# Optimization experiments

Hardware: AMD Instinct MI355X
Metric: run time of the kernel (lower is better)

## Reference

```python
import jax, jax.numpy as jnp
import numpy as np

IN_FEATURES = 512
OUT_FEATURES = 512
BATCH = 1024


def setup_inputs() -> dict:
    key = jax.random.key(0)
    k_x, k_w = jax.random.split(key)
    X = jax.random.normal(k_x, (BATCH, IN_FEATURES), dtype=jnp.float32)
    # xavier_uniform init for W [out, in]: U(-a, a), a = sqrt(6/(fan_in+fan_out))
    a = np.sqrt(6.0 / (IN_FEATURES + OUT_FEATURES)).astype(np.float32)
    W = jax.random.uniform(k_w, (OUT_FEATURES, IN_FEATURES), dtype=jnp.float32,
                           minval=-a, maxval=a)
    return {"X": X, "W": W}


def reference(X, W):
    # Tropical (min-plus) linear layer:
    #   out[b, o] = min_i ( X[b, i] + W[o, i] )
    # Broadcast-add produces [B, O, I], then min-reduce over in_features.
    return jnp.min(X[:, None, :] + W[None, :, :], axis=-1)
```

## Files before the change

### kernel.cpp

```cpp
#include <hip/hip_runtime.h>
#include <math.h>


#define B_SZ  1024
#define O_F   512
#define I_F   512
#define MB    8
#define NO    4
#define NTHR  256

typedef __attribute__((ext_vector_type(4))) float f32x4;

__global__ __launch_bounds__(NTHR, 4)
void tropical_v5(const float* __restrict__ X,
                 const float* __restrict__ W,
                 float* __restrict__ out) {
  __shared__ f32x4 Xs[16 * 128];

  const int tid  = threadIdx.x;
  const int wv   = tid >> 6;
  const int lane = tid & 63;
  const int k16  = lane & 15;
  const int og   = lane >> 4;

  const int bid = blockIdx.x;
  const int swz = (bid & 7) * 128 + (bid >> 3);
  const int ot  = swz >> 6;
  const int bt  = swz & 63;
  const int b0b = bt * 16;
  const int o0  = ot * 32 + (wv & 1) * 16;
  const int bw  = (wv >> 1) * 8;

  const f32x4* __restrict__ Xv = reinterpret_cast<const f32x4*>(X);
  const f32x4* __restrict__ Wv = reinterpret_cast<const f32x4*>(W);
  const int R4 = I_F / 4;

#pragma unroll
  for (int it = 0; it < 8; ++it) {
    const int slot0 = (wv * 8 + it) * 64;
    const int f     = slot0 + lane;
    const f32x4* src = &Xv[(size_t)(b0b + (f >> 7)) * R4 + (f & 127)];
    __builtin_amdgcn_global_load_lds(
        (const __attribute__((address_space(1))) void*)src,
        (__attribute__((address_space(3))) void*)&Xs[slot0],
        16, 0, 0);
  }
  __syncthreads();

  float acc[MB][NO];
#pragma unroll
  for (int m = 0; m < MB; ++m)
#pragma unroll
    for (int n = 0; n < NO; ++n) acc[m][n] = __builtin_inff();

#pragma unroll
  for (int c = 0; c < I_F / 64; ++c) {
    const int k4 = c * 16 + k16;
    f32x4 x4[MB];
#pragma unroll
    for (int m = 0; m < MB; ++m)
      x4[m] = Xs[(bw + m) * 128 + k4];
#pragma unroll
    for (int n = 0; n < NO; ++n) {
      const f32x4 w4 = Wv[(size_t)(o0 + n * 4 + og) * R4 + k4];
#pragma unroll
      for (int m = 0; m < MB; ++m) {
        float c0 = x4[m].x + w4.x;
        float c1 = x4[m].y + w4.y;
        float c2 = x4[m].z + w4.z;
        float c3 = x4[m].w + w4.w;
        acc[m][n] = fminf(fminf(c0, c1), acc[m][n]);
        acc[m][n] = fminf(fminf(c2, c3), acc[m][n]);
      }
    }
  }

  float v0[32];
#pragma unroll
  for (int m = 0; m < MB; ++m)
#pragma unroll
    for (int n = 0; n < NO; ++n) v0[(m << 2) | n] = acc[m][n];

  const bool bb0 = (k16 & 1);
  float v1[16];
#pragma unroll
  for (int i = 0; i < 16; ++i) {
    float keep = bb0 ? v0[2 * i + 1] : v0[2 * i];
    float send = bb0 ? v0[2 * i]     : v0[2 * i + 1];
    v1[i] = fminf(keep, __shfl_xor(send, 1, 64));
  }
  const bool bb1 = (k16 >> 1) & 1;
  float v2[8];
#pragma unroll
  for (int i = 0; i < 8; ++i) {
    float keep = bb1 ? v1[2 * i + 1] : v1[2 * i];
    float send = bb1 ? v1[2 * i]     : v1[2 * i + 1];
    v2[i] = fminf(keep, __shfl_xor(send, 2, 64));
  }
  const bool bb2 = (k16 >> 2) & 1;
  float v3[4];
#pragma unroll
  for (int i = 0; i < 4; ++i) {
    float keep = bb2 ? v2[2 * i + 1] : v2[2 * i];
    float send = bb2 ? v2[2 * i]     : v2[2 * i + 1];
    v3[i] = fminf(keep, __shfl_xor(send, 4, 64));
  }
  const bool bb3 = (k16 >> 3) & 1;
  float v4[2];
#pragma unroll
  for (int i = 0; i < 2; ++i) {
    float keep = bb3 ? v3[2 * i + 1] : v3[2 * i];
    float send = bb3 ? v3[2 * i]     : v3[2 * i + 1];
    v4[i] = fminf(keep, __shfl_xor(send, 8, 64));
  }

  const int mrow = k16 >> 2;
  const int ncol = k16 & 3;
#pragma unroll
  for (int h = 0; h < 2; ++h) {
    out[(size_t)(b0b + bw + 4 * h + mrow) * O_F + o0 + 4 * ncol + og] = v4[h];
  }
}

extern "C" void kernel_launch(void* const* d_in, const int* in_sizes, int n_in,
                              void* d_out, int out_size, void* d_ws, size_t ws_size,
                              hipStream_t stream) {
  const float* X = (const float*)d_in[0];
  const float* W = (const float*)d_in[1];
  float* out     = (float*)d_out;

  hipLaunchKernelGGL(tropical_v5, dim3(1024), dim3(NTHR), 0, stream,
                     X, W, out);
}
```

Before: 17.96 us.

## Convert inputs to fp16 and compute min-plus with packed half instructions

Adds a pre-pass kernel that converts X and W to fp16 in the workspace, then runs the main kernel on fp16 data using packed add and v_pk_min_f16, so each instruction handles two elements. This halves memory and LDS traffic and doubles the ALU throughput of the inner loop. The cost is an extra kernel launch plus the conversion pass, and fp16 rounding of the inputs and sums may exceed the reference tolerance.

```diff
diff --git a/kernel.cpp b/kernel.cpp
--- a/kernel.cpp
+++ b/kernel.cpp
@@ -8,14 +8,47 @@
 #define MB    8
 #define NO    4
 #define NTHR  256
+#define XN    (B_SZ * I_F)
+#define WN    (O_F * I_F)
 
-typedef __attribute__((ext_vector_type(4))) float f32x4;
+typedef __attribute__((ext_vector_type(4))) float    f32x4;
+typedef __attribute__((ext_vector_type(8))) _Float16 f16x8;
+typedef __attribute__((ext_vector_type(2))) _Float16 h2;
+
+template <int J>
+static __device__ __forceinline__ h2 pair_of(f16x8 v) {
+  return __builtin_shufflevector(v, v, 2 * J, 2 * J + 1);
+}
+
+static __device__ __forceinline__ h2 pkmin(h2 a, h2 b) {
+  h2 r;
+  asm("v_pk_min_f16 %0, %1, %2" : "=v"(r) : "v"(a), "v"(b));
+  return r;
+}
+
+__global__ __launch_bounds__(NTHR, 8)
+void cvt_f16(const float* __restrict__ X, const float* __restrict__ W,
+             f16x8* __restrict__ dst) {
+  const int t = blockIdx.x * NTHR + threadIdx.x;
+  const f32x4* __restrict__ Xv = reinterpret_cast<const f32x4*>(X);
+  const f32x4* __restrict__ Wv = reinterpret_cast<const f32x4*>(W);
+  f32x4 a, b;
+  if (t < XN / 8) { a = Xv[2 * t];              b = Xv[2 * t + 1]; }
+  else            { const int u = t - XN / 8;
+                    a = Wv[2 * u];              b = Wv[2 * u + 1]; }
+  f16x8 h;
+  h[0] = (_Float16)a.x; h[1] = (_Float16)a.y;
+  h[2] = (_Float16)a.z; h[3] = (_Float16)a.w;
+  h[4] = (_Float16)b.x; h[5] = (_Float16)b.y;
+  h[6] = (_Float16)b.z; h[7] = (_Float16)b.w;
+  dst[t] = h;
+}
 
 __global__ __launch_bounds__(NTHR, 4)
-void tropical_v5(const float* __restrict__ X,
-                 const float* __restrict__ W,
+void tropical_v9(const f16x8* __restrict__ Xh,
+                 const f16x8* __restrict__ Wh,
                  float* __restrict__ out) {
-  __shared__ f32x4 Xs[16 * 128];
+  __shared__ f16x8 Xs[16 * 64];
 
   const int tid  = threadIdx.x;
   const int wv   = tid >> 6;
@@ -29,17 +62,13 @@
   const int bt  = swz & 63;
   const int b0b = bt * 16;
   const int o0  = ot * 32 + (wv & 1) * 16;
-  const int bw  = (wv >> 1) * 8;
-
-  const f32x4* __restrict__ Xv = reinterpret_cast<const f32x4*>(X);
-  const f32x4* __restrict__ Wv = reinterpret_cast<const f32x4*>(W);
-  const int R4 = I_F / 4;
+  const int bw  = (wv >> 1) * MB;
 
 #pragma unroll
-  for (int it = 0; it < 8; ++it) {
-    const int slot0 = (wv * 8 + it) * 64;
+  for (int it = 0; it < 4; ++it) {
+    const int slot0 = (wv * 4 + it) * 64;
     const int f     = slot0 + lane;
-    const f32x4* src = &Xv[(size_t)(b0b + (f >> 7)) * R4 + (f & 127)];
+    const f16x8* src = &Xh[(size_t)(b0b + (f >> 6)) * 64 + (f & 63)];
     __builtin_amdgcn_global_load_lds(
         (const __attribute__((address_space(1))) void*)src,
         (__attribute__((address_space(3))) void*)&Xs[slot0],
@@ -47,30 +76,35 @@
   }
   __syncthreads();
 
-  float acc[MB][NO];
+  const _Float16 hinf = (_Float16)__builtin_inff();
+  h2 acc2[MB][NO];
 #pragma unroll
   for (int m = 0; m < MB; ++m)
 #pragma unroll
-    for (int n = 0; n < NO; ++n) acc[m][n] = __builtin_inff();
+    for (int n = 0; n < NO; ++n) acc2[m][n] = (h2){hinf, hinf};
 
 #pragma unroll
-  for (int c = 0; c < I_F / 64; ++c) {
-    const int k4 = c * 16 + k16;
-    f32x4 x4[MB];
+  for (int c = 0; c < 4; ++c) {
+    const int slot = c * 16 + k16;
+    f16x8 x8[MB];
 #pragma unroll
     for (int m = 0; m < MB; ++m)
-      x4[m] = Xs[(bw + m) * 128 + k4];
+      x8[m] = Xs[(bw + m) * 64 + slot];
 #pragma unroll
     for (int n = 0; n < NO; ++n) {
-      const f32x4 w4 = Wv[(size_t)(o0 + n * 4 + og) * R4 + k4];
+      const f16x8 w8 = Wh[(size_t)(o0 + n * 4 + og) * 64 + slot];
+      const h2 w0 = pair_of<0>(w8), w1 = pair_of<1>(w8),
+               w2 = pair_of<2>(w8), w3 = pair_of<3>(w8);
 #pragma unroll
       for (int m = 0; m < MB; ++m) {
-        float c0 = x4[m].x + w4.x;
-        float c1 = x4[m].y + w4.y;
-        float c2 = x4[m].z + w4.z;
-        float c3 = x4[m].w + w4.w;
-        acc[m][n] = fminf(fminf(c0, c1), acc[m][n]);
-        acc[m][n] = fminf(fminf(c2, c3), acc[m][n]);
+        const h2 s0 = pair_of<0>(x8[m]) + w0;
+        acc2[m][n] = pkmin(acc2[m][n], s0);
+        const h2 s1 = pair_of<1>(x8[m]) + w1;
+        acc2[m][n] = pkmin(acc2[m][n], s1);
+        const h2 s2 = pair_of<2>(x8[m]) + w2;
+        acc2[m][n] = pkmin(acc2[m][n], s2);
+        const h2 s3 = pair_of<3>(x8[m]) + w3;
+        acc2[m][n] = pkmin(acc2[m][n], s3);
       }
     }
   }
@@ -79,7 +113,8 @@
 #pragma unroll
   for (int m = 0; m < MB; ++m)
 #pragma unroll
-    for (int n = 0; n < NO; ++n) v0[(m << 2) | n] = acc[m][n];
+    for (int n = 0; n < NO; ++n)
+      v0[(m << 2) | n] = fminf((float)acc2[m][n][0], (float)acc2[m][n][1]);
 
   const bool bb0 = (k16 & 1);
   float v1[16];
@@ -129,6 +164,11 @@
   const float* W = (const float*)d_in[1];
   float* out     = (float*)d_out;
 
-  hipLaunchKernelGGL(tropical_v5, dim3(1024), dim3(NTHR), 0, stream,
-                     X, W, out);
+  f16x8* Xh = (f16x8*)d_ws;
+  f16x8* Wh = Xh + XN / 8;
+
+  hipLaunchKernelGGL(cvt_f16, dim3((XN + WN) / 8 / NTHR), dim3(NTHR), 0,
+                     stream, X, W, Xh);
+  hipLaunchKernelGGL(tropical_v9, dim3(1024), dim3(NTHR), 0, stream,
+                     Xh, Wh, out);
 }
```

Result: slower. 24.45 us (+36.1%).
